# Kernel optimization log

Hardware: AMD Instinct MI355X
Metric: run time of the kernel (lower is better)

## Reference

```python
import jax, jax.numpy as jnp
import numpy as np

LN2 = float(np.log(2.0))
CUTOFF_L = 0.5


def _ssp(x):
    # shifted softplus: log(0.5*exp(x) + 0.5)
    return jax.nn.softplus(x) - LN2


def _pair_idx(n):
    # ordered pairs arranged [n, n-1]: for each i, all j != i
    idx = np.arange(n)
    j = np.stack([np.concatenate([idx[:k], idx[k + 1:]]) for k in range(n)])  # [n, n-1]
    i = np.broadcast_to(idx[:, None], j.shape)
    return jnp.asarray(i), jnp.asarray(j)


def _mlp3(x, w1, b1, w2, b2, w3, b3):
    h = _ssp(x @ w1 + b1)
    h = _ssp(h @ w2 + b2)
    return h @ w3 + b3


def _backflow_cutoff(r, L=CUTOFF_L):
    r = r / L
    return jnp.where(r < L, r ** 2 * (6.0 - 8.0 * r + 3.0 * r ** 2), jnp.ones((), r.dtype))


def setup_inputs() -> dict:
    key = jax.random.key(0)
    ks = jax.random.split(key, 12)
    B, N, D, K = 512, 32, 256, 8
    dims_e = [D, 40, 6, 1]
    dims_n = [D, 81, 25, 8]

    def lin(k, fi, fo):
        return jax.random.normal(k, (fi, fo), jnp.float32) / np.sqrt(fi)

    inp = {
        'rs': jax.random.normal(ks[0], (B, N, 3), jnp.float32),
        'xs': jax.random.normal(ks[1], (B, N, D), jnp.float32),
        'coords': jax.random.normal(ks[2], (K, 3), jnp.float32) * 2.0,
        'ew1': lin(ks[3], dims_e[0], dims_e[1]), 'eb1': jnp.zeros((dims_e[1],), jnp.float32),
        'ew2': lin(ks[4], dims_e[1], dims_e[2]), 'eb2': jnp.zeros((dims_e[2],), jnp.float32),
        'ew3': lin(ks[5], dims_e[2], dims_e[3]), 'eb3': jnp.zeros((dims_e[3],), jnp.float32),
        'nw1': lin(ks[6], dims_n[0], dims_n[1]), 'nb1': jnp.zeros((dims_n[1],), jnp.float32),
        'nw2': lin(ks[7], dims_n[1], dims_n[2]), 'nb2': jnp.zeros((dims_n[2],), jnp.float32),
        'nw3': lin(ks[8], dims_n[2], dims_n[3]), 'nb3': jnp.zeros((dims_n[3],), jnp.float32),
    }
    return inp


def reference(rs, xs, coords, ew1, eb1, ew2, eb2, ew3, eb3,
              nw1, nb1, nw2, nb2, nw3, nb3):
    n_elec = rs.shape[-2]
    i, j = _pair_idx(n_elec)  # [n, n-1] static index arrays

    # electron-electron backflow
    diffs_elec = rs[..., i, :] - rs[..., j, :]                    # [B, n, n-1, 3]
    pair_feat = xs[..., i, :] * xs[..., j, :]                     # [B, n, n-1, D]
    w_pair = _mlp3(pair_feat, ew1, eb1, ew2, eb2, ew3, eb3)       # [B, n, n-1, 1]
    bf_elec = (w_pair * diffs_elec).sum(axis=-2)                  # [B, n, 3]

    # electron-nucleus backflow
    diffs_nuc = rs[..., :, None, :] - coords                      # [B, n, K, 3]
    w_nuc = _mlp3(xs, nw1, nb1, nw2, nb2, nw3, nb3)               # [B, n, K]
    bf_nuc = (w_nuc[..., None] * diffs_nuc).sum(axis=-2)          # [B, n, 3]

    dist_nuc = jnp.linalg.norm(diffs_nuc, axis=-1)                # [B, n, K]
    cutoff = _backflow_cutoff(dist_nuc).prod(axis=-1)             # [B, n]

    return rs + 1e-4 * cutoff[..., None] * (bf_elec + bf_nuc)
```

## Files before the change

### kernel.cpp

```cpp
#include <hip/hip_runtime.h>
#include <stdint.h>

static constexpr int B_ = 512, N_ = 32, D_ = 256, K_ = 8;
static constexpr int E1 = 40, E2 = 6;
static constexpr int N1 = 81, N2 = 25, N3 = 8;
static constexpr int XBP = 264;
static constexpr int H1P = 72;
static constexpr int HEP = 88;
static constexpr int EWT = 264;
static constexpr int TKP = 40;
static constexpr float LN2f  = 0.69314718055994530942f;
static constexpr float L2Ef  = 1.44269504088896340736f;

typedef float    f32x4 __attribute__((ext_vector_type(4)));
typedef _Float16 f16x8 __attribute__((ext_vector_type(8)));

__device__ __forceinline__ float sspf(float x) {
    float t = __builtin_amdgcn_exp2f(x * L2Ef);
    return LN2f * __builtin_amdgcn_logf(fmaf(t, 0.5f, 0.5f));
}

__global__ __launch_bounds__(512) void k_fused(
    const float* __restrict__ rs, const float* __restrict__ xs,
    const float* __restrict__ coords,
    const float* __restrict__ ew1, const float* __restrict__ eb1,
    const float* __restrict__ ew2, const float* __restrict__ eb2,
    const float* __restrict__ ew3, const float* __restrict__ eb3,
    const float* __restrict__ nw1, const float* __restrict__ nb1,
    const float* __restrict__ nw2, const float* __restrict__ nb2,
    const float* __restrict__ nw3, const float* __restrict__ nb3,
    float* __restrict__ out)
{
    __shared__ alignas(16) _Float16 xs_h[N_ * XBP];
    __shared__ alignas(16) _Float16 wbuf[E1 * EWT];
    __shared__ alignas(16) char uni[8 * 16 * H1P * 2];
    __shared__ float w_s[N_ * N_];
    __shared__ float nw2_s[N1 * N2];
    __shared__ float nw3_s[N2 * N3];
    __shared__ float rs_s[N_ * 3];
    __shared__ float nb2_s[N2];
    __shared__ float nb3_s[N3];
    __shared__ float co_s[K_ * 3];
    __shared__ float bfn_s[N_ * 3];
    __shared__ float cut_s[N_];

    _Float16* h1e = (_Float16*)uni;
    float*    h2e = (float*)(uni + N_ * HEP * 2);

    const int b = blockIdx.x, t = threadIdx.x;
    const int wv = t >> 6, l = t & 63, quad = l >> 4, c = l & 15;

    f16x8 b2f[2];
    #pragma unroll
    for (int Kt = 0; Kt < 2; ++Kt) {
        union { uint32_t d[4]; f16x8 v; } f;
        #pragma unroll
        for (int d2 = 0; d2 < 4; ++d2) {
            int k0 = Kt * 32 + quad * 8 + 2 * d2;
            union { _Float16 h[2]; uint32_t u; } pk;
            pk.h[0] = (_Float16)((k0 < E1 && c < E2) ? ew2[k0 * E2 + c] : 0.f);
            pk.h[1] = (_Float16)((k0 + 1 < E1 && c < E2) ? ew2[(k0 + 1) * E2 + c] : 0.f);
            f.d[d2] = pk.u;
        }
        b2f[Kt] = f.v;
    }
    float eb1v[3];
    #pragma unroll
    for (int Nt = 0; Nt < 3; ++Nt) { int n = Nt * 16 + c; eb1v[Nt] = (n < E1) ? eb1[n] : 0.f; }
    const float eb2v = (c < E2) ? eb2[c] : 0.f;
    const float w3v  = (c < E2) ? ew3[c] : 0.f;
    const float eb3v = eb3[0];
    float nb1v[2];
    #pragma unroll
    for (int e = 0; e < 2; ++e) {
        int p = wv + 8 * e, n = (p >> 1) * 16 + c;
        nb1v[e] = (p < 12 && n < N1) ? nb1[n] : 0.f;
    }

    {
        const float4* src = (const float4*)(xs + (size_t)b * N_ * D_);
        #pragma unroll
        for (int u = 0; u < 4; ++u) {
            int q = t + 512 * u;
            float4 v = src[q];
            int row = q >> 6, col4 = q & 63;
            union { _Float16 h[4]; uint64_t u64; } pk;
            pk.h[0] = (_Float16)v.x; pk.h[1] = (_Float16)v.y;
            pk.h[2] = (_Float16)v.z; pk.h[3] = (_Float16)v.w;
            *(uint64_t*)&xs_h[row * XBP + col4 * 4] = pk.u64;
        }
    }
    {
        const float4* src = (const float4*)ew1;
        #pragma unroll
        for (int u = 0; u < 5; ++u) {
            int q = t + 512 * u;
            float4 v = src[q];
            int k = q / 10, n0 = (q - 10 * k) * 4;
            wbuf[(n0 + 0) * EWT + k] = (_Float16)v.x;
            wbuf[(n0 + 1) * EWT + k] = (_Float16)v.y;
            wbuf[(n0 + 2) * EWT + k] = (_Float16)v.z;
            wbuf[(n0 + 3) * EWT + k] = (_Float16)v.w;
        }
    }
    if (t < N_ * 3) rs_s[t] = rs[b * N_ * 3 + t];
    for (int i2 = t; i2 < N1 * N2; i2 += 512) nw2_s[i2] = nw2[i2];
    if (t < N2 * N3) nw3_s[t] = nw3[t];
    if (t < N2) nb2_s[t] = nb2[t];
    if (t < N3) nb3_s[t] = nb3[t];
    if (t < K_ * 3) co_s[t] = coords[t];
    __syncthreads();

    f16x8 b1f[3][8];
    #pragma unroll
    for (int Nt = 0; Nt < 3; ++Nt) {
        int n = Nt * 16 + c;
        bool ok = (n < E1);
        int row = ok ? n : 0;
        #pragma unroll
        for (int Kt = 0; Kt < 8; ++Kt) {
            f16x8 v = *(const f16x8*)&wbuf[row * EWT + Kt * 32 + quad * 8];
            if (!ok) v = (f16x8)(_Float16)0.f;
            b1f[Nt][Kt] = v;
        }
    }
    __syncthreads();

    {
        f32x4 acc3[2];
        #pragma unroll
        for (int e = 0; e < 2; ++e) acc3[e] = (f32x4){0.f, 0.f, 0.f, 0.f};

        {
            const float* wk = nw1;
            #pragma unroll
            for (int u = 0; u < 6; ++u) {
                int idx = t + 512 * u;
                int n = idx >> 5, k = idx & 31;
                float v = (n < N1) ? wk[k * N1 + n] : 0.f;
                wbuf[n * TKP + k] = (_Float16)v;
            }
        }
        __syncthreads();
        #pragma unroll 1
        for (int Kt = 0; Kt < 8; ++Kt) {
            if (Kt < 7) {
                const float* wk = nw1 + ((Kt + 1) * 32) * N1;
                _Float16* dst = wbuf + ((Kt + 1) & 1) * (96 * TKP);
                #pragma unroll
                for (int u = 0; u < 6; ++u) {
                    int idx = t + 512 * u;
                    int n = idx >> 5, k = idx & 31;
                    float v = (n < N1) ? wk[k * N1 + n] : 0.f;
                    dst[n * TKP + k] = (_Float16)v;
                }
            }
            const _Float16* T = wbuf + (Kt & 1) * (96 * TKP);
            #pragma unroll
            for (int e = 0; e < 2; ++e) {
                int p = wv + 8 * e;
                if (p < 12) {
                    int Mt = p & 1, Nt = p >> 1;
                    f16x8 A  = *(const f16x8*)&xs_h[(Mt * 16 + c) * XBP + Kt * 32 + quad * 8];
                    f16x8 Bf = *(const f16x8*)&T[(Nt * 16 + c) * TKP + quad * 8];
                    acc3[e] = __builtin_amdgcn_mfma_f32_16x16x32_f16(A, Bf, acc3[e], 0, 0, 0);
                }
            }
            __syncthreads();
        }
        #pragma unroll
        for (int e = 0; e < 2; ++e) {
            int p = wv + 8 * e;
            if (p < 12) {
                int Mt = p & 1, Nt = p >> 1;
                int n = Nt * 16 + c;
                if (n < N1) {
                    #pragma unroll
                    for (int r2 = 0; r2 < 4; ++r2) {
                        int m = Mt * 16 + quad * 4 + r2;
                        h1e[m * HEP + n] = (_Float16)sspf(acc3[e][r2] + nb1v[e]);
                    }
                }
            }
        }
    }
    __syncthreads();

    {
        const int r = t >> 4, s = t & 15;
        const int n0 = 2 * s;
        if (n0 < N2) {
            float a0 = 0.f, a1 = 0.f;
            const int rb = r * HEP;
            for (int kk = 0; kk < N1; ++kk) {
                float hv = (float)h1e[rb + kk];
                const float* wrow = nw2_s + kk * N2 + n0;
                a0 = fmaf(hv, wrow[0], a0);
                if (n0 + 1 < N2) a1 = fmaf(hv, wrow[1], a1);
            }
            h2e[r * 26 + n0] = sspf(a0 + nb2_s[n0]);
            if (n0 + 1 < N2) h2e[r * 26 + n0 + 1] = sspf(a1 + nb2_s[n0 + 1]);
        }
    }
    __syncthreads();

    if (t < 256) {
        const int r = t >> 3, s = t & 7;
        float w = nb3_s[s];
        const int rb = r * 26;
        #pragma unroll
        for (int kk = 0; kk < N2; ++kk)
            w = fmaf(h2e[rb + kk], nw3_s[kk * N3 + s], w);

        float dx = rs_s[r * 3 + 0] - co_s[s * 3 + 0];
        float dy = rs_s[r * 3 + 1] - co_s[s * 3 + 1];
        float dz = rs_s[r * 3 + 2] - co_s[s * 3 + 2];
        float cx = w * dx, cy = w * dy, cz = w * dz;
        #pragma unroll
        for (int m2 = 1; m2 < 8; m2 <<= 1) {
            cx += __shfl_xor(cx, m2);
            cy += __shfl_xor(cy, m2);
            cz += __shfl_xor(cz, m2);
        }
        float rr  = sqrtf(dx * dx + dy * dy + dz * dz);
        float xsc = 2.f * rr;
        float cf  = (xsc < 0.5f) ? xsc * xsc * (6.f - 8.f * xsc + 3.f * xsc * xsc) : 1.f;
        #pragma unroll
        for (int m2 = 1; m2 < 8; m2 <<= 1) cf *= __shfl_xor(cf, m2);
        if (s == 0) {
            bfn_s[r * 3 + 0] = cx;
            bfn_s[r * 3 + 1] = cy;
            bfn_s[r * 3 + 2] = cz;
            cut_s[r] = cf;
        }
    }
    __syncthreads();

    _Float16* myh1 = (_Float16*)(uni + wv * (16 * H1P * 2));
    *(uint64_t*)&myh1[c * H1P + 48 + quad * 4] = 0ull;

    #pragma unroll 1
    for (int q8 = 0; q8 < 4; ++q8) {
        const int i = wv + 8 * q8;
        f32x4 acc[2][3];
        #pragma unroll
        for (int h = 0; h < 2; ++h)
            #pragma unroll
            for (int Nt = 0; Nt < 3; ++Nt) acc[h][Nt] = (f32x4){0.f, 0.f, 0.f, 0.f};

        #pragma unroll
        for (int Kt = 0; Kt < 8; ++Kt) {
            const int koff = Kt * 32 + quad * 8;
            f16x8 iv  = *(const f16x8*)&xs_h[i * XBP + koff];
            f16x8 jv0 = *(const f16x8*)&xs_h[c * XBP + koff];
            f16x8 jv1 = *(const f16x8*)&xs_h[(16 + c) * XBP + koff];
            f16x8 A0 = iv * jv0;
            f16x8 A1 = iv * jv1;
            #pragma unroll
            for (int Nt = 0; Nt < 3; ++Nt) {
                acc[0][Nt] = __builtin_amdgcn_mfma_f32_16x16x32_f16(A0, b1f[Nt][Kt], acc[0][Nt], 0, 0, 0);
                acc[1][Nt] = __builtin_amdgcn_mfma_f32_16x16x32_f16(A1, b1f[Nt][Kt], acc[1][Nt], 0, 0, 0);
            }
        }

        #pragma unroll
        for (int h = 0; h < 2; ++h) {
            #pragma unroll
            for (int Nt = 0; Nt < 3; ++Nt) {
                #pragma unroll
                for (int r2 = 0; r2 < 4; ++r2) {
                    float hv = sspf(acc[h][Nt][r2] + eb1v[Nt]);
                    myh1[(quad * 4 + r2) * H1P + Nt * 16 + c] = (_Float16)hv;
                }
            }
            f32x4 acc2 = {0.f, 0.f, 0.f, 0.f};
            #pragma unroll
            for (int Kt2 = 0; Kt2 < 2; ++Kt2) {
                f16x8 a2 = *(const f16x8*)&myh1[c * H1P + Kt2 * 32 + quad * 8];
                acc2 = __builtin_amdgcn_mfma_f32_16x16x32_f16(a2, b2f[Kt2], acc2, 0, 0, 0);
            }
            float wp[4];
            #pragma unroll
            for (int r2 = 0; r2 < 4; ++r2) wp[r2] = sspf(acc2[r2] + eb2v) * w3v;
            #pragma unroll
            for (int m2 = 1; m2 < 16; m2 <<= 1) {
                #pragma unroll
                for (int r2 = 0; r2 < 4; ++r2) wp[r2] += __shfl_xor(wp[r2], m2);
            }
            if (c == 0) {
                int Mt = 2 * i + h;
                float4* dst = (float4*)&w_s[Mt * 16 + quad * 4];
                *dst = make_float4(wp[0] + eb3v, wp[1] + eb3v, wp[2] + eb3v, wp[3] + eb3v);
            }
        }
    }
    __syncthreads();

    if (t < 256) {
        const int i = t >> 3, si = t & 7;
        const float4 wq = *(const float4*)&w_s[i * 32 + si * 4];
        const float rix = rs_s[i * 3 + 0], riy = rs_s[i * 3 + 1], riz = rs_s[i * 3 + 2];
        float cx = 0.f, cy = 0.f, cz = 0.f;
        const float wa[4] = {wq.x, wq.y, wq.z, wq.w};
        #pragma unroll
        for (int u = 0; u < 4; ++u) {
            int j = si * 4 + u;
            cx = fmaf(wa[u], rix - rs_s[j * 3 + 0], cx);
            cy = fmaf(wa[u], riy - rs_s[j * 3 + 1], cy);
            cz = fmaf(wa[u], riz - rs_s[j * 3 + 2], cz);
        }
        #pragma unroll
        for (int m2 = 1; m2 < 8; m2 <<= 1) {
            cx += __shfl_xor(cx, m2);
            cy += __shfl_xor(cy, m2);
            cz += __shfl_xor(cz, m2);
        }
        if (si < 3) {
            float bfe = (si == 0) ? cx : ((si == 1) ? cy : cz);
            int idx = i * 3 + si;
            out[(size_t)b * (N_ * 3) + idx] =
                rs_s[idx] + 1e-4f * cut_s[i] * (bfe + bfn_s[idx]);
        }
    }
}

extern "C" void kernel_launch(void* const* d_in, const int* in_sizes, int n_in,
                              void* d_out, int out_size, void* d_ws, size_t ws_size,
                              hipStream_t stream)
{
    const float* rs     = (const float*)d_in[0];
    const float* xs     = (const float*)d_in[1];
    const float* coords = (const float*)d_in[2];
    const float* ew1    = (const float*)d_in[3];
    const float* eb1    = (const float*)d_in[4];
    const float* ew2    = (const float*)d_in[5];
    const float* eb2    = (const float*)d_in[6];
    const float* ew3    = (const float*)d_in[7];
    const float* eb3    = (const float*)d_in[8];
    const float* nw1    = (const float*)d_in[9];
    const float* nb1    = (const float*)d_in[10];
    const float* nw2    = (const float*)d_in[11];
    const float* nb2    = (const float*)d_in[12];
    const float* nw3    = (const float*)d_in[13];
    const float* nb3    = (const float*)d_in[14];

    k_fused<<<B_, 512, 0, stream>>>(rs, xs, coords, ew1, eb1, ew2, eb2, ew3, eb3,
                                    nw1, nb1, nw2, nb2, nw3, nb3, (float*)d_out);
}
```

Measured before the change: 154.1 us.

## Register-prefetch nucleus weights, swizzle LDS tiles, fuse electron backflow reduction in-wave

The nucleus-MLP first-layer weights are now prefetched into registers one K-tile ahead and written to LDS at the top of each iteration, with an XOR swizzle and a padded row stride meant to cut bank conflicts. The write-then-sync order keeps a single barrier per iteration. The per-pair weights are folded straight into per-electron backflow sums in registers and reduced with cross-quad shuffles, which removes the w_s buffer and its extra pass. It also adds a launch_bounds occupancy hint, which may limit registers and cause spills.

```diff
diff --git a/kernel.cpp b/kernel.cpp
--- a/kernel.cpp
+++ b/kernel.cpp
@@ -8,19 +8,20 @@
 static constexpr int H1P = 72;
 static constexpr int HEP = 88;
 static constexpr int EWT = 264;
-static constexpr int TKP = 40;
+static constexpr int TKP = 44;
 static constexpr float LN2f  = 0.69314718055994530942f;
 static constexpr float L2Ef  = 1.44269504088896340736f;
 
 typedef float    f32x4 __attribute__((ext_vector_type(4)));
 typedef _Float16 f16x8 __attribute__((ext_vector_type(8)));
+typedef _Float16 f16x4 __attribute__((ext_vector_type(4)));
 
 __device__ __forceinline__ float sspf(float x) {
     float t = __builtin_amdgcn_exp2f(x * L2Ef);
     return LN2f * __builtin_amdgcn_logf(fmaf(t, 0.5f, 0.5f));
 }
 
-__global__ __launch_bounds__(512) void k_fused(
+__global__ __launch_bounds__(512, 4) void k_fused(
     const float* __restrict__ rs, const float* __restrict__ xs,
     const float* __restrict__ coords,
     const float* __restrict__ ew1, const float* __restrict__ eb1,
@@ -34,7 +35,6 @@
     __shared__ alignas(16) _Float16 xs_h[N_ * XBP];
     __shared__ alignas(16) _Float16 wbuf[E1 * EWT];
     __shared__ alignas(16) char uni[8 * 16 * H1P * 2];
-    __shared__ float w_s[N_ * N_];
     __shared__ float nw2_s[N1 * N2];
     __shared__ float nw3_s[N2 * N3];
     __shared__ float rs_s[N_ * 3];
@@ -43,6 +43,7 @@
     __shared__ float co_s[K_ * 3];
     __shared__ float bfn_s[N_ * 3];
     __shared__ float cut_s[N_];
+    __shared__ float bfe_s[N_ * 3];
 
     _Float16* h1e = (_Float16*)uni;
     float*    h2e = (float*)(uni + N_ * HEP * 2);
@@ -124,6 +125,14 @@
             b1f[Nt][Kt] = v;
         }
     }
+
+    float pf[6];
+    #pragma unroll
+    for (int u = 0; u < 6; ++u) {
+        int idx = t + 512 * u;
+        int k = idx / 96, n = idx - 96 * k;
+        pf[u] = (n < N1) ? nw1[k * N1 + n] : 0.f;
+    }
     __syncthreads();
 
     {
@@ -131,43 +140,43 @@
         #pragma unroll
         for (int e = 0; e < 2; ++e) acc3[e] = (f32x4){0.f, 0.f, 0.f, 0.f};
 
-        {
-            const float* wk = nw1;
+        #pragma unroll 1
+        for (int Kt = 0; Kt < 8; ++Kt) {
+            _Float16* dst = wbuf + (Kt & 1) * (96 * TKP);
             #pragma unroll
             for (int u = 0; u < 6; ++u) {
                 int idx = t + 512 * u;
-                int n = idx >> 5, k = idx & 31;
-                float v = (n < N1) ? wk[k * N1 + n] : 0.f;
-                wbuf[n * TKP + k] = (_Float16)v;
-            }
-        }
-        __syncthreads();
-        #pragma unroll 1
-        for (int Kt = 0; Kt < 8; ++Kt) {
+                int k = idx / 96, n = idx - 96 * k;
+                int ks = k ^ (((n >> 4) & 1) << 3);
+                dst[n * TKP + ks] = (_Float16)pf[u];
+            }
             if (Kt < 7) {
                 const float* wk = nw1 + ((Kt + 1) * 32) * N1;
-                _Float16* dst = wbuf + ((Kt + 1) & 1) * (96 * TKP);
                 #pragma unroll
                 for (int u = 0; u < 6; ++u) {
                     int idx = t + 512 * u;
-                    int n = idx >> 5, k = idx & 31;
-                    float v = (n < N1) ? wk[k * N1 + n] : 0.f;
-                    dst[n * TKP + k] = (_Float16)v;
+                    int k = idx / 96, n = idx - 96 * k;
+                    pf[u] = (n < N1) ? wk[k * N1 + n] : 0.f;
                 }
             }
+            __syncthreads();
             const _Float16* T = wbuf + (Kt & 1) * (96 * TKP);
             #pragma unroll
             for (int e = 0; e < 2; ++e) {
                 int p = wv + 8 * e;
                 if (p < 12) {
                     int Mt = p & 1, Nt = p >> 1;
-                    f16x8 A  = *(const f16x8*)&xs_h[(Mt * 16 + c) * XBP + Kt * 32 + quad * 8];
-                    f16x8 Bf = *(const f16x8*)&T[(Nt * 16 + c) * TKP + quad * 8];
+                    f16x8 A = *(const f16x8*)&xs_h[(Mt * 16 + c) * XBP + Kt * 32 + quad * 8];
+                    int rb = (Nt * 16 + c) * TKP;
+                    int kb = (quad * 8) ^ ((Nt & 1) << 3);
+                    f16x4 lo = *(const f16x4*)&T[rb + kb];
+                    f16x4 hi = *(const f16x4*)&T[rb + kb + 4];
+                    f16x8 Bf = __builtin_shufflevector(lo, hi, 0, 1, 2, 3, 4, 5, 6, 7);
                     acc3[e] = __builtin_amdgcn_mfma_f32_16x16x32_f16(A, Bf, acc3[e], 0, 0, 0);
                 }
             }
-            __syncthreads();
-        }
+        }
+        __syncthreads();
         #pragma unroll
         for (int e = 0; e < 2; ++e) {
             int p = wv + 8 * e;
@@ -263,6 +272,8 @@
             }
         }
 
+        const float rix = rs_s[i * 3 + 0], riy = rs_s[i * 3 + 1], riz = rs_s[i * 3 + 2];
+        float cxi = 0.f, cyi = 0.f, czi = 0.f;
         #pragma unroll
         for (int h = 0; h < 2; ++h) {
             #pragma unroll
@@ -287,40 +298,33 @@
                 #pragma unroll
                 for (int r2 = 0; r2 < 4; ++r2) wp[r2] += __shfl_xor(wp[r2], m2);
             }
-            if (c == 0) {
-                int Mt = 2 * i + h;
-                float4* dst = (float4*)&w_s[Mt * 16 + quad * 4];
-                *dst = make_float4(wp[0] + eb3v, wp[1] + eb3v, wp[2] + eb3v, wp[3] + eb3v);
-            }
-        }
-    }
-    __syncthreads();
-
-    if (t < 256) {
-        const int i = t >> 3, si = t & 7;
-        const float4 wq = *(const float4*)&w_s[i * 32 + si * 4];
-        const float rix = rs_s[i * 3 + 0], riy = rs_s[i * 3 + 1], riz = rs_s[i * 3 + 2];
-        float cx = 0.f, cy = 0.f, cz = 0.f;
-        const float wa[4] = {wq.x, wq.y, wq.z, wq.w};
-        #pragma unroll
-        for (int u = 0; u < 4; ++u) {
-            int j = si * 4 + u;
-            cx = fmaf(wa[u], rix - rs_s[j * 3 + 0], cx);
-            cy = fmaf(wa[u], riy - rs_s[j * 3 + 1], cy);
-            cz = fmaf(wa[u], riz - rs_s[j * 3 + 2], cz);
-        }
-        #pragma unroll
-        for (int m2 = 1; m2 < 8; m2 <<= 1) {
-            cx += __shfl_xor(cx, m2);
-            cy += __shfl_xor(cy, m2);
-            cz += __shfl_xor(cz, m2);
-        }
-        if (si < 3) {
-            float bfe = (si == 0) ? cx : ((si == 1) ? cy : cz);
-            int idx = i * 3 + si;
-            out[(size_t)b * (N_ * 3) + idx] =
-                rs_s[idx] + 1e-4f * cut_s[i] * (bfe + bfn_s[idx]);
-        }
+            #pragma unroll
+            for (int r2 = 0; r2 < 4; ++r2) {
+                int j = quad * 4 + r2 + 16 * h;
+                float wj = wp[r2] + eb3v;
+                cxi = fmaf(wj, rix - rs_s[j * 3 + 0], cxi);
+                cyi = fmaf(wj, riy - rs_s[j * 3 + 1], cyi);
+                czi = fmaf(wj, riz - rs_s[j * 3 + 2], czi);
+            }
+        }
+        #pragma unroll
+        for (int m2 = 16; m2 < 64; m2 <<= 1) {
+            cxi += __shfl_xor(cxi, m2);
+            cyi += __shfl_xor(cyi, m2);
+            czi += __shfl_xor(czi, m2);
+        }
+        if (l == 0) {
+            bfe_s[i * 3 + 0] = cxi;
+            bfe_s[i * 3 + 1] = cyi;
+            bfe_s[i * 3 + 2] = czi;
+        }
+    }
+    __syncthreads();
+
+    if (t < N_ * 3) {
+        int i = t / 3;
+        out[(size_t)b * (N_ * 3) + t] =
+            rs_s[t] + 1e-4f * cut_s[i] * (bfe_s[t] + bfn_s[t]);
     }
 }
 
```

After: 193.6 us. +25.6%, slower.
